# Performance work log

Hardware: AMD Instinct MI355X
Metric: run time of the kernel (lower is better)

The kernel has to match this reference:

```python
import jax, jax.numpy as jnp
import numpy as np

N_SITES = 1024
N_SYMM = 1024
ALPHA_SYMM = 16  # alpha * n_sites / n_symm with alpha=16


def logcosh(x):
    # numerically stable log(cosh(x)) = |x| + log1p(exp(-2|x|)) - log(2)
    ax = jnp.abs(x)
    return ax + jnp.log1p(jnp.exp(-2.0 * ax)) - jnp.log(2.0)


def setup_inputs() -> dict:
    key = jax.random.key(0)
    k1, k2, k3, k4 = jax.random.split(key, 4)
    x_in = jax.random.normal(k1, (4096, N_SITES), dtype=jnp.float32)
    Wsymm = jax.random.normal(k2, (N_SITES, ALPHA_SYMM), dtype=jnp.float32) * 0.1
    bsymm = jax.random.normal(k3, (ALPHA_SYMM,), dtype=jnp.float32) * 0.1
    v_bias = jax.random.normal(k4, (1,), dtype=jnp.float32) * 0.1
    # cyclic translation group: perm_i[k] = (k + i) mod n_sites
    perms = (np.arange(N_SITES)[:, None] + np.arange(N_SITES)[None, :]) % N_SITES
    perms = jnp.asarray(perms, dtype=jnp.int32)  # [n_symm, n_sites]
    return {"x_in": x_in, "Wsymm": Wsymm, "bsymm": bsymm, "v_bias": v_bias, "perms": perms}


def reference(x_in, Wsymm, bsymm, v_bias, perms):
    n_symm, n_sites = perms.shape
    # expand_kernel: kernel[i, j*n_sites + k] = Wsymm[perms[i, k], j]
    # Wsymm[perms] -> [n_symm, n_sites, alpha_symm]; transpose and flatten -> [n_symm, alpha_symm*n_sites]
    kernel = jnp.transpose(Wsymm[perms], (0, 2, 1)).reshape(n_symm, -1)
    # expand_bias: repeat each bsymm[j] n_symm times -> [alpha_symm*n_symm]
    bias = jnp.repeat(bsymm, n_symm)
    y = x_in @ kernel + bias  # [batch, n_hidden]
    y = jnp.sum(logcosh(y), axis=-1)  # [batch]
    y = y + v_bias[0] * jnp.sum(x_in, axis=-1)
    return y
```

## Files before the change

kernel.cpp:

```cpp
#include <hip/hip_runtime.h>
#include <hip/hip_bf16.h>
#include <math.h>

#define LN2F 0.6931471805599453f
#define SCL 9.765625e-4f

typedef __attribute__((ext_vector_type(2))) float f32x2;


#define LSW(s) ((s) ^ (((s) >> 4) & 15))

__device__ __forceinline__ f32x2 mk2(float x, float y) { f32x2 r; r.x = x; r.y = y; return r; }
__device__ __forceinline__ f32x2 crot(f32x2 d) { return mk2(-d.y, d.x); }
__device__ __forceinline__ f32x2 cmul(f32x2 a, f32x2 b) {
  return a.xx * b + mk2(-a.y, a.y) * b.yx;
}
__device__ __forceinline__ f32x2 cmulj(f32x2 a, f32x2 b) {
  return b.xx * a + mk2(b.y, -b.y) * a.yx;
}

__device__ __forceinline__ f32x2 Ctw(int m) {
  switch (m) {
    case 0:   return mk2(1.f, 0.f);
    case 1:   return mk2(0.999981175f, -0.006135885f);
    case 2:   return mk2(0.999924702f, -0.012271538f);
    case 3:   return mk2(0.999830582f, -0.018406730f);
    case 64:  return mk2(0.923879533f, -0.382683432f);
    case 128: return mk2(0.707106781f, -0.707106781f);
    case 192: return mk2(0.382683432f, -0.923879533f);
    case 256: return mk2(0.f, -1.f);
    case 384: return mk2(-0.707106781f, -0.707106781f);
    case 576: return mk2(-0.923879533f, 0.382683432f);
  }
  return mk2(1.f, 0.f);
}

#define BFLY_F(x0,x1,x2,x3,W1,W2,W3,y0,y1,y2,y3) do { \
  f32x2 t0 = x0+x2, t1 = x1+x3, t2 = x0-x2, d_ = x1-x3; \
  f32x2 t3 = mk2(d_.y, -d_.x); \
  y0 = t0+t1; y1 = cmul(t2+t3, W1); \
  y2 = cmul(t0-t1, W2); y3 = cmul(t2-t3, W3); } while(0)

#define BFLY_I(x0,x1,x2,x3,W1,W2,W3,y0,y1,y2,y3) do { \
  f32x2 u1 = cmulj(x1,W1), u2 = cmulj(x2,W2), u3 = cmulj(x3,W3); \
  f32x2 t0 = x0+u2, t1 = u1+u3, t2 = x0-u2, d_ = u1-u3; \
  f32x2 t3 = mk2(-d_.y, d_.x); \
  y0 = t0+t1; y1 = t2+t3; y2 = t0-t1; y3 = t2-t3; } while(0)

#define BFLY_I1(x0,x1,x2,x3,y0,y1,y2,y3) do { \
  f32x2 t0 = x0+x2, t1 = x1+x3, t2 = x0-x2, d_ = x1-x3; \
  f32x2 t3 = mk2(-d_.y, d_.x); \
  y0 = t0+t1; y1 = t2+t3; y2 = t0-t1; y3 = t2-t3; } while(0)

__device__ __forceinline__ float lc(float v) {
  float a = fabsf(v);
  return a + __logf(1.f + __expf(-2.f * a));
}

__global__ void k_twiddle(f32x2* __restrict__ tw) {
  int m = blockIdx.x * 256 + threadIdx.x;
  float th = (float)(2.0 * M_PI / 1024.0) * (float)m;
  tw[m] = mk2(cosf(th), -sinf(th));
}

__global__ __launch_bounds__(256, 3) void k_fft_fwd(
    const float* __restrict__ src, int estride, int rstride,
    const f32x2* __restrict__ tw, f32x2* __restrict__ dst,
    const float* __restrict__ vbias, float* __restrict__ out, int dorow) {
  __shared__ __align__(16) f32x2 fft[4][1024];
  int tid = threadIdx.x, wv = tid >> 6, u = tid & 63;
  int row = blockIdx.x * 4 + wv;
  const float* xr = src + (size_t)row * rstride;
  f32x2* L = fft[wv];
  f32x2 twu = tw[u];
  f32x2 tw4u = tw[4 * u];
  int tp = u & 3;
  f32x2 tw16t = tw[16 * tp], tw64t = tw[64 * tp];

  float vr[4][4]; float rs = 0.f;
  #pragma unroll
  for (int a = 0; a < 4; ++a)
    #pragma unroll
    for (int k = 0; k < 4; ++k) {
      float s = xr[(u + 64 * a + 256 * k) * estride];
      vr[a][k] = s; rs += s;
    }
  f32x2 v[4][4];
  #pragma unroll
  for (int a = 0; a < 4; ++a) {
    float x0 = vr[a][0], x1 = vr[a][1], x2 = vr[a][2], x3 = vr[a][3];
    float t0 = x0 + x2, t1 = x1 + x3, t2 = x0 - x2, dm = x1 - x3;
    f32x2 W1 = cmul(twu, Ctw(64 * a));
    f32x2 W2 = cmul(W1, W1), W3 = cmul(W1, W2);
    v[a][0] = mk2(t0 + t1, 0.f);
    v[a][1] = cmul(mk2(t2, -dm), W1);
    v[a][2] = cmul(mk2(t0 - t1, 0.f), W2);
    v[a][3] = cmul(mk2(t2, dm), W3);
  }
  {
    f32x2 W1 = tw4u, W2 = cmul(W1, W1), W3 = cmul(W1, W2);
    #pragma unroll
    for (int k = 0; k < 4; ++k) {
      f32x2 y0,y1,y2,y3;
      BFLY_F(v[0][k], v[1][k], v[2][k], v[3][k], W1, W2, W3, y0,y1,y2,y3);
      v[0][k]=y0; v[1][k]=y1; v[2][k]=y2; v[3][k]=y3;
    }
  }
  #pragma unroll
  for (int a = 0; a < 4; ++a)
    #pragma unroll
    for (int k = 0; k < 4; ++k)
      L[LSW(u + 64 * a + 256 * k)] = v[a][k];

  int D = u >> 2;
  f32x2 w[4][4];
  #pragma unroll
  for (int c = 0; c < 4; ++c)
    #pragma unroll
    for (int ap = 0; ap < 4; ++ap)
      w[c][ap] = L[LSW(64 * D + 16 * c + 4 * ap + tp)];
  #pragma unroll
  for (int ap = 0; ap < 4; ++ap) {
    f32x2 W1 = cmul(Ctw(64 * ap), tw16t);
    f32x2 W2 = cmul(W1, W1), W3 = cmul(W1, W2);
    f32x2 y0,y1,y2,y3;
    BFLY_F(w[0][ap], w[1][ap], w[2][ap], w[3][ap], W1, W2, W3, y0,y1,y2,y3);
    w[0][ap]=y0; w[1][ap]=y1; w[2][ap]=y2; w[3][ap]=y3;
  }
  {
    f32x2 W1 = tw64t, W2 = cmul(W1, W1), W3 = cmul(W1, W2);
    #pragma unroll
    for (int c = 0; c < 4; ++c) {
      f32x2 y0,y1,y2,y3;
      BFLY_F(w[c][0], w[c][1], w[c][2], w[c][3], W1, W2, W3, y0,y1,y2,y3);
      w[c][0]=y0; w[c][1]=y1; w[c][2]=y2; w[c][3]=y3;
    }
  }
  #pragma unroll
  for (int c = 0; c < 4; ++c)
    #pragma unroll
    for (int ap = 0; ap < 4; ++ap)
      L[LSW(64 * D + 16 * c + 4 * ap + tp)] = w[c][ap];

  f32x2* drow = dst + (size_t)row * 1024;
  #pragma unroll
  for (int j = 0; j < 4; ++j) {
    f32x2 z0 = L[LSW(16 * u + 4 * j)];
    f32x2 z1 = L[LSW(16 * u + 4 * j + 1)];
    f32x2 z2 = L[LSW(16 * u + 4 * j + 2)];
    f32x2 z3 = L[LSW(16 * u + 4 * j + 3)];
    f32x2 t0 = z0+z2, t1 = z1+z3, t2 = z0-z2, d = z1-z3;
    f32x2 t3 = mk2(d.y, -d.x);
    f32x2 y0 = t0+t1, y1 = t2+t3, y2 = t0-t1, y3 = t2-t3;
    float4* dp = (float4*)(drow + 16 * u + 4 * j);
    dp[0] = make_float4(y0.x, y0.y, y1.x, y1.y);
    dp[1] = make_float4(y2.x, y2.y, y3.x, y3.y);
  }
  if (dorow) {
    #pragma unroll
    for (int m = 32; m; m >>= 1) rs += __shfl_down(rs, m);
    if (u == 0) out[row] = vbias[0] * rs;
  }
}


#define PW(M, XA, XB, ZA, ZB) do { \
  float4 qa = W0p[M], qb = W1p[M]; \
  f32x2 g1 = cmulj(mk2(qa.x,qa.y), XA); \
  f32x2 g2 = cmulj(mk2(qb.x,qb.y), XA); \
  ZA = (g1 + crot(g2)) * SCL; \
  g1 = cmulj(mk2(qa.z,qa.w), XB); \
  g2 = cmulj(mk2(qb.z,qb.w), XB); \
  ZB = (g1 + crot(g2)) * SCL; } while(0)

#define QP_A(P, LB) do { \
  const float4* W0p = (const float4*)(Wfs + (size_t)(2*(P)) * 1024 + s16); \
  const float4* W1p = (const float4*)(Wfs + (size_t)(2*(P) + 1) * 1024 + s16); \
  f32x2 z0,z1,z2,z3,z4,z5,z6,z7,z8,z9,z10,z11,z12,z13,z14,z15; \
  PW(0, xr0, xr1, z0, z1);   PW(1, xr2, xr3, z2, z3); \
  PW(2, xr4, xr5, z4, z5);   PW(3, xr6, xr7, z6, z7); \
  PW(4, xr8, xr9, z8, z9);   PW(5, xr10, xr11, z10, z11); \
  PW(6, xr12, xr13, z12, z13); PW(7, xr14, xr15, z14, z15); \
   \
  BFLY_I1(z0,z1,z2,z3, z0,z1,z2,z3); \
  BFLY_I1(z4,z5,z6,z7, z4,z5,z6,z7); \
  BFLY_I1(z8,z9,z10,z11, z8,z9,z10,z11); \
  BFLY_I1(z12,z13,z14,z15, z12,z13,z14,z15); \
   \
  BFLY_I1(z0,z4,z8,z12, z0,z4,z8,z12); \
  BFLY_I(z1,z5,z9,z13, Ctw(64),Ctw(128),Ctw(192), z1,z5,z9,z13); \
  BFLY_I(z2,z6,z10,z14, Ctw(128),Ctw(256),Ctw(384), z2,z6,z10,z14); \
  BFLY_I(z3,z7,z11,z15, Ctw(192),Ctw(384),Ctw(576), z3,z7,z11,z15); \
  (LB)[LSW(s16+0)]=z0;   (LB)[LSW(s16+1)]=z1;   (LB)[LSW(s16+2)]=z2;   (LB)[LSW(s16+3)]=z3; \
  (LB)[LSW(s16+4)]=z4;   (LB)[LSW(s16+5)]=z5;   (LB)[LSW(s16+6)]=z6;   (LB)[LSW(s16+7)]=z7; \
  (LB)[LSW(s16+8)]=z8;   (LB)[LSW(s16+9)]=z9;   (LB)[LSW(s16+10)]=z10; (LB)[LSW(s16+11)]=z11; \
  (LB)[LSW(s16+12)]=z12; (LB)[LSW(s16+13)]=z13; (LB)[LSW(s16+14)]=z14; (LB)[LSW(s16+15)]=z15; \
} while(0)

#define QP_B(LB) do { \
  f32x2 w00,w01,w02,w03,w10,w11,w12,w13,w20,w21,w22,w23,w30,w31,w32,w33; \
  w00 = (LB)[LSW(sB+0)];   w01 = (LB)[LSW(sB+64)];  w02 = (LB)[LSW(sB+128)]; w03 = (LB)[LSW(sB+192)]; \
  w10 = (LB)[LSW(sB+16)];  w11 = (LB)[LSW(sB+80)];  w12 = (LB)[LSW(sB+144)]; w13 = (LB)[LSW(sB+208)]; \
  w20 = (LB)[LSW(sB+32)];  w21 = (LB)[LSW(sB+96)];  w22 = (LB)[LSW(sB+160)]; w23 = (LB)[LSW(sB+224)]; \
  w30 = (LB)[LSW(sB+48)];  w31 = (LB)[LSW(sB+112)]; w32 = (LB)[LSW(sB+176)]; w33 = (LB)[LSW(sB+240)]; \
  BFLY_I(w00,w10,w20,w30, TB1,TB2,TB3, w00,w10,w20,w30); \
  BFLY_I(w01,w11,w21,w31, TB1,TB2,TB3, w01,w11,w21,w31); \
  BFLY_I(w02,w12,w22,w32, TB1,TB2,TB3, w02,w12,w22,w32); \
  BFLY_I(w03,w13,w23,w33, TB1,TB2,TB3, w03,w13,w23,w33); \
  BFLY_I(w00,w01,w02,w03, TC10,TC20,TC30, w00,w01,w02,w03); \
  BFLY_I(w10,w11,w12,w13, TC11,TC21,TC31, w10,w11,w12,w13); \
  BFLY_I(w20,w21,w22,w23, TC12,TC22,TC32, w20,w21,w22,w23); \
  BFLY_I(w30,w31,w32,w33, TC13,TC23,TC33, w30,w31,w32,w33); \
  (LB)[LSW(sB+0)]=w00;   (LB)[LSW(sB+64)]=w01;  (LB)[LSW(sB+128)]=w02; (LB)[LSW(sB+192)]=w03; \
  (LB)[LSW(sB+16)]=w10;  (LB)[LSW(sB+80)]=w11;  (LB)[LSW(sB+144)]=w12; (LB)[LSW(sB+208)]=w13; \
  (LB)[LSW(sB+32)]=w20;  (LB)[LSW(sB+96)]=w21;  (LB)[LSW(sB+160)]=w22; (LB)[LSW(sB+224)]=w23; \
  (LB)[LSW(sB+48)]=w30;  (LB)[LSW(sB+112)]=w31; (LB)[LSW(sB+176)]=w32; (LB)[LSW(sB+240)]=w33; \
} while(0)

#define QPC_PH(LB, I, T1, T2, T3, BS0, BS1) do { \
  f32x2 c0 = (LB)[LSW(s4+(I))],     c1 = (LB)[LSW(s4+(I)+256)]; \
  f32x2 c2 = (LB)[LSW(s4+(I)+512)], c3 = (LB)[LSW(s4+(I)+768)]; \
  BFLY_I(c0,c1,c2,c3,T1,T2,T3,c0,c1,c2,c3); \
  a0 += lc(c0.x+(BS0)) + lc(c0.y+(BS1)); \
  a1 += lc(c1.x+(BS0)) + lc(c1.y+(BS1)); \
  a2 += lc(c2.x+(BS0)) + lc(c2.y+(BS1)); \
  a3 += lc(c3.x+(BS0)) + lc(c3.y+(BS1)); } while(0)

#define QP_C(LB, BS0, BS1) do { \
  QPC_PH(LB, 0, TD10, TD20, TD30, BS0, BS1); \
  QPC_PH(LB, 1, TD11, TD21, TD31, BS0, BS1); \
  QPC_PH(LB, 2, TD12, TD22, TD32, BS0, BS1); \
  QPC_PH(LB, 3, TD13, TD23, TD33, BS0, BS1); } while(0)

__global__ __launch_bounds__(512, 4) void k_corr(
    const f32x2* __restrict__ X, const f32x2* __restrict__ Wfs,
    const float* __restrict__ bs, const f32x2* __restrict__ tw,
    float* __restrict__ out) {
  __shared__ __align__(16) f32x2 LBW[8][1024];
  __shared__ float red[8];
  int tid = threadIdx.x, wv = tid >> 6, u = tid & 63;
  int b = blockIdx.x;
  f32x2* L0 = LBW[wv];
  f32x2 tw4u = tw[4 * u];
  int t = u & 15;
  f32x2 tw16t = tw[16 * t], tw4t = tw[4 * t];
  int s16 = 16 * u;
  int sB = 256 * (u >> 4) + t;
  int s4 = 4 * u;

  f32x2 xr0,xr1,xr2,xr3,xr4,xr5,xr6,xr7,xr8,xr9,xr10,xr11,xr12,xr13,xr14,xr15;
  {
    const float4* Xp = (const float4*)(X + (size_t)b * 1024 + s16);
    float4 q;
    q = Xp[0]; xr0  = mk2(q.x,q.y); xr1  = mk2(q.z,q.w);
    q = Xp[1]; xr2  = mk2(q.x,q.y); xr3  = mk2(q.z,q.w);
    q = Xp[2]; xr4  = mk2(q.x,q.y); xr5  = mk2(q.z,q.w);
    q = Xp[3]; xr6  = mk2(q.x,q.y); xr7  = mk2(q.z,q.w);
    q = Xp[4]; xr8  = mk2(q.x,q.y); xr9  = mk2(q.z,q.w);
    q = Xp[5]; xr10 = mk2(q.x,q.y); xr11 = mk2(q.z,q.w);
    q = Xp[6]; xr12 = mk2(q.x,q.y); xr13 = mk2(q.z,q.w);
    q = Xp[7]; xr14 = mk2(q.x,q.y); xr15 = mk2(q.z,q.w);
  }
  float bs0 = bs[2*wv], bs1 = bs[2*wv+1];

  QP_A(wv, L0);

  f32x2 TB1 = tw16t, TB2 = cmul(TB1,TB1), TB3 = cmul(TB1,TB2);
  f32x2 TC10 = tw4t,               TC20 = cmul(TC10,TC10), TC30 = cmul(TC10,TC20);
  f32x2 TC11 = cmul(tw4t,Ctw(64)),  TC21 = cmul(TC11,TC11), TC31 = cmul(TC11,TC21);
  f32x2 TC12 = cmul(tw4t,Ctw(128)), TC22 = cmul(TC12,TC12), TC32 = cmul(TC12,TC22);
  f32x2 TC13 = cmul(tw4t,Ctw(192)), TC23 = cmul(TC13,TC13), TC33 = cmul(TC13,TC23);

  QP_B(L0);

  f32x2 TD10 = tw4u,              TD20 = cmul(TD10,TD10), TD30 = cmul(TD10,TD20);
  f32x2 TD11 = cmul(tw4u,Ctw(1)), TD21 = cmul(TD11,TD11), TD31 = cmul(TD11,TD21);
  f32x2 TD12 = cmul(tw4u,Ctw(2)), TD22 = cmul(TD12,TD12), TD32 = cmul(TD12,TD22);
  f32x2 TD13 = cmul(tw4u,Ctw(3)), TD23 = cmul(TD13,TD13), TD33 = cmul(TD13,TD23);

  float a0 = 0.f, a1 = 0.f, a2 = 0.f, a3 = 0.f;
  QP_C(L0, bs0, bs1);

  float acc = (a0 + a1) + (a2 + a3);
  #pragma unroll
  for (int m = 32; m; m >>= 1) acc += __shfl_down(acc, m);
  if (u == 0) red[wv] = acc;
  __syncthreads();
  if (tid == 0) {
    float s = ((red[0] + red[1]) + (red[2] + red[3]))
            + ((red[4] + red[5]) + (red[6] + red[7]));
    out[b] += s - 16384.f * LN2F;
  }
}

__global__ void k_naive(const float* __restrict__ x, const float* __restrict__ W,
                        const float* __restrict__ bs, const float* __restrict__ vb,
                        float* __restrict__ out) {
  int b = blockIdx.x;
  __shared__ float xs[1024];
  __shared__ float red[256];
  int t = threadIdx.x;
  float xsum = 0.f;
  for (int i = t; i < 1024; i += 256) { float v = x[(size_t)b * 1024 + i]; xs[i] = v; xsum += v; }
  __syncthreads();
  float tot = vb[0] * xsum;
  for (int h = t; h < 16384; h += 256) {
    int j = h >> 10, kh = h & 1023;
    float a = bs[j];
    for (int i = 0; i < 1024; ++i) a += xs[i] * W[((i + kh) & 1023) * 16 + j];
    float ax = fabsf(a);
    tot += ax + __logf(1.f + __expf(-2.f * ax)) - LN2F;
  }
  red[t] = tot;
  __syncthreads();
  for (int s2 = 128; s2; s2 >>= 1) { if (t < s2) red[t] += red[t + s2]; __syncthreads(); }
  if (t == 0) out[b] = red[0];
}

extern "C" void kernel_launch(void* const* d_in, const int* in_sizes, int n_in,
                              void* d_out, int out_size, void* d_ws, size_t ws_size,
                              hipStream_t stream) {
  const float* x  = (const float*)d_in[0];
  const float* W  = (const float*)d_in[1];
  const float* bs = (const float*)d_in[2];
  const float* vb = (const float*)d_in[3];
  float* out = (float*)d_out;

  size_t need = 8192 + 131072 + (size_t)4096 * 1024 * 8;
  if (ws_size < need) {
    k_naive<<<4096, 256, 0, stream>>>(x, W, bs, vb, out);
    return;
  }
  f32x2* tw  = (f32x2*)d_ws;
  f32x2* Wfs = (f32x2*)((char*)d_ws + 8192);
  f32x2* X   = (f32x2*)((char*)d_ws + 8192 + 131072);

  k_twiddle<<<4, 256, 0, stream>>>(tw);
  k_fft_fwd<<<4, 256, 0, stream>>>(W, 16, 1, tw, Wfs, vb, out, 0);
  k_fft_fwd<<<1024, 256, 0, stream>>>(x, 1, 1024, tw, X, vb, out, 1);
  k_corr<<<4096, 512, 0, stream>>>(X, Wfs, bs, tw, out);
}
```

Measured before the change: 138.5 us.

## Pad LDS layout, fold FFT scale into W, and use log2-domain logcosh

Replaces the XOR-swizzled LDS indexing in the correlation kernel with a padded layout (row stride 17/272, plus a u>>2 offset) and precomputed per-lane base pointers, which removes the per-access swizzle arithmetic. The 1/1024 inverse-FFT scale moves into the one-time W spectrum kernel, taking a multiply off every pointwise product. logcosh is rewritten in base 2 using a packed abs via max, a vector accumulator for the linear term and a single ln2 factor at the end. This cuts per-element ALU work, at the cost of more shared memory per block and slightly different rounding.

```diff
diff --git a/kernel.cpp b/kernel.cpp
--- a/kernel.cpp
+++ b/kernel.cpp
@@ -4,6 +4,7 @@
 
 #define LN2F 0.6931471805599453f
 #define SCL 9.765625e-4f
+#define TWO_OVER_LN2 2.885390081777927f
 
 typedef __attribute__((ext_vector_type(2))) float f32x2;
 
@@ -17,6 +18,13 @@
 }
 __device__ __forceinline__ f32x2 cmulj(f32x2 a, f32x2 b) {
   return b.xx * a + mk2(b.y, -b.y) * a.yx;
+}
+__device__ __forceinline__ f32x2 vmax2(f32x2 a, f32x2 b) {
+#if __has_builtin(__builtin_elementwise_max)
+  return __builtin_elementwise_max(a, b);
+#else
+  return mk2(fmaxf(a.x, b.x), fmaxf(a.y, b.y));
+#endif
 }
 
 __device__ __forceinline__ f32x2 Ctw(int m) {
@@ -52,11 +60,6 @@
   f32x2 t3 = mk2(-d_.y, d_.x); \
   y0 = t0+t1; y1 = t2+t3; y2 = t0-t1; y3 = t2-t3; } while(0)
 
-__device__ __forceinline__ float lc(float v) {
-  float a = fabsf(v);
-  return a + __logf(1.f + __expf(-2.f * a));
-}
-
 __global__ void k_twiddle(f32x2* __restrict__ tw) {
   int m = blockIdx.x * 256 + threadIdx.x;
   float th = (float)(2.0 * M_PI / 1024.0) * (float)m;
@@ -65,7 +68,7 @@
 
 __global__ __launch_bounds__(256, 3) void k_fft_fwd(
     const float* __restrict__ src, int estride, int rstride,
-    const f32x2* __restrict__ tw, f32x2* __restrict__ dst,
+    const f32x2* __restrict__ tw, f32x2* __restrict__ dst, float scale,
     const float* __restrict__ vbias, float* __restrict__ out, int dorow) {
   __shared__ __align__(16) f32x2 fft[4][1024];
   int tid = threadIdx.x, wv = tid >> 6, u = tid & 63;
@@ -151,7 +154,7 @@
     f32x2 z3 = L[LSW(16 * u + 4 * j + 3)];
     f32x2 t0 = z0+z2, t1 = z1+z3, t2 = z0-z2, d = z1-z3;
     f32x2 t3 = mk2(d.y, -d.x);
-    f32x2 y0 = t0+t1, y1 = t2+t3, y2 = t0-t1, y3 = t2-t3;
+    f32x2 y0 = (t0+t1)*scale, y1 = (t2+t3)*scale, y2 = (t0-t1)*scale, y3 = (t2-t3)*scale;
     float4* dp = (float4*)(drow + 16 * u + 4 * j);
     dp[0] = make_float4(y0.x, y0.y, y1.x, y1.y);
     dp[1] = make_float4(y2.x, y2.y, y3.x, y3.y);
@@ -168,12 +171,12 @@
   float4 qa = W0p[M], qb = W1p[M]; \
   f32x2 g1 = cmulj(mk2(qa.x,qa.y), XA); \
   f32x2 g2 = cmulj(mk2(qb.x,qb.y), XA); \
-  ZA = (g1 + crot(g2)) * SCL; \
+  ZA = g1 + crot(g2); \
   g1 = cmulj(mk2(qa.z,qa.w), XB); \
   g2 = cmulj(mk2(qb.z,qb.w), XB); \
-  ZB = (g1 + crot(g2)) * SCL; } while(0)
-
-#define QP_A(P, LB) do { \
+  ZB = g1 + crot(g2); } while(0)
+
+#define QP_A(P, LPA) do { \
   const float4* W0p = (const float4*)(Wfs + (size_t)(2*(P)) * 1024 + s16); \
   const float4* W1p = (const float4*)(Wfs + (size_t)(2*(P) + 1) * 1024 + s16); \
   f32x2 z0,z1,z2,z3,z4,z5,z6,z7,z8,z9,z10,z11,z12,z13,z14,z15; \
@@ -181,28 +184,26 @@
   PW(2, xr4, xr5, z4, z5);   PW(3, xr6, xr7, z6, z7); \
   PW(4, xr8, xr9, z8, z9);   PW(5, xr10, xr11, z10, z11); \
   PW(6, xr12, xr13, z12, z13); PW(7, xr14, xr15, z14, z15); \
-   \
   BFLY_I1(z0,z1,z2,z3, z0,z1,z2,z3); \
   BFLY_I1(z4,z5,z6,z7, z4,z5,z6,z7); \
   BFLY_I1(z8,z9,z10,z11, z8,z9,z10,z11); \
   BFLY_I1(z12,z13,z14,z15, z12,z13,z14,z15); \
-   \
   BFLY_I1(z0,z4,z8,z12, z0,z4,z8,z12); \
   BFLY_I(z1,z5,z9,z13, Ctw(64),Ctw(128),Ctw(192), z1,z5,z9,z13); \
   BFLY_I(z2,z6,z10,z14, Ctw(128),Ctw(256),Ctw(384), z2,z6,z10,z14); \
   BFLY_I(z3,z7,z11,z15, Ctw(192),Ctw(384),Ctw(576), z3,z7,z11,z15); \
-  (LB)[LSW(s16+0)]=z0;   (LB)[LSW(s16+1)]=z1;   (LB)[LSW(s16+2)]=z2;   (LB)[LSW(s16+3)]=z3; \
-  (LB)[LSW(s16+4)]=z4;   (LB)[LSW(s16+5)]=z5;   (LB)[LSW(s16+6)]=z6;   (LB)[LSW(s16+7)]=z7; \
-  (LB)[LSW(s16+8)]=z8;   (LB)[LSW(s16+9)]=z9;   (LB)[LSW(s16+10)]=z10; (LB)[LSW(s16+11)]=z11; \
-  (LB)[LSW(s16+12)]=z12; (LB)[LSW(s16+13)]=z13; (LB)[LSW(s16+14)]=z14; (LB)[LSW(s16+15)]=z15; \
+  (LPA)[0]=z0;   (LPA)[1]=z1;   (LPA)[2]=z2;   (LPA)[3]=z3; \
+  (LPA)[4]=z4;   (LPA)[5]=z5;   (LPA)[6]=z6;   (LPA)[7]=z7; \
+  (LPA)[8]=z8;   (LPA)[9]=z9;   (LPA)[10]=z10; (LPA)[11]=z11; \
+  (LPA)[12]=z12; (LPA)[13]=z13; (LPA)[14]=z14; (LPA)[15]=z15; \
 } while(0)
 
-#define QP_B(LB) do { \
+#define QP_B(LPB) do { \
   f32x2 w00,w01,w02,w03,w10,w11,w12,w13,w20,w21,w22,w23,w30,w31,w32,w33; \
-  w00 = (LB)[LSW(sB+0)];   w01 = (LB)[LSW(sB+64)];  w02 = (LB)[LSW(sB+128)]; w03 = (LB)[LSW(sB+192)]; \
-  w10 = (LB)[LSW(sB+16)];  w11 = (LB)[LSW(sB+80)];  w12 = (LB)[LSW(sB+144)]; w13 = (LB)[LSW(sB+208)]; \
-  w20 = (LB)[LSW(sB+32)];  w21 = (LB)[LSW(sB+96)];  w22 = (LB)[LSW(sB+160)]; w23 = (LB)[LSW(sB+224)]; \
-  w30 = (LB)[LSW(sB+48)];  w31 = (LB)[LSW(sB+112)]; w32 = (LB)[LSW(sB+176)]; w33 = (LB)[LSW(sB+240)]; \
+  w00 = (LPB)[0];   w01 = (LPB)[68];  w02 = (LPB)[136]; w03 = (LPB)[204]; \
+  w10 = (LPB)[17];  w11 = (LPB)[85];  w12 = (LPB)[153]; w13 = (LPB)[221]; \
+  w20 = (LPB)[34];  w21 = (LPB)[102]; w22 = (LPB)[170]; w23 = (LPB)[238]; \
+  w30 = (LPB)[51];  w31 = (LPB)[119]; w32 = (LPB)[187]; w33 = (LPB)[255]; \
   BFLY_I(w00,w10,w20,w30, TB1,TB2,TB3, w00,w10,w20,w30); \
   BFLY_I(w01,w11,w21,w31, TB1,TB2,TB3, w01,w11,w21,w31); \
   BFLY_I(w02,w12,w22,w32, TB1,TB2,TB3, w02,w12,w22,w32); \
@@ -211,42 +212,48 @@
   BFLY_I(w10,w11,w12,w13, TC11,TC21,TC31, w10,w11,w12,w13); \
   BFLY_I(w20,w21,w22,w23, TC12,TC22,TC32, w20,w21,w22,w23); \
   BFLY_I(w30,w31,w32,w33, TC13,TC23,TC33, w30,w31,w32,w33); \
-  (LB)[LSW(sB+0)]=w00;   (LB)[LSW(sB+64)]=w01;  (LB)[LSW(sB+128)]=w02; (LB)[LSW(sB+192)]=w03; \
-  (LB)[LSW(sB+16)]=w10;  (LB)[LSW(sB+80)]=w11;  (LB)[LSW(sB+144)]=w12; (LB)[LSW(sB+208)]=w13; \
-  (LB)[LSW(sB+32)]=w20;  (LB)[LSW(sB+96)]=w21;  (LB)[LSW(sB+160)]=w22; (LB)[LSW(sB+224)]=w23; \
-  (LB)[LSW(sB+48)]=w30;  (LB)[LSW(sB+112)]=w31; (LB)[LSW(sB+176)]=w32; (LB)[LSW(sB+240)]=w33; \
+  (LPB)[0]=w00;   (LPB)[68]=w01;  (LPB)[136]=w02; (LPB)[204]=w03; \
+  (LPB)[17]=w10;  (LPB)[85]=w11;  (LPB)[153]=w12; (LPB)[221]=w13; \
+  (LPB)[34]=w20;  (LPB)[102]=w21; (LPB)[170]=w22; (LPB)[238]=w23; \
+  (LPB)[51]=w30;  (LPB)[119]=w31; (LPB)[187]=w32; (LPB)[255]=w33; \
 } while(0)
 
-#define QPC_PH(LB, I, T1, T2, T3, BS0, BS1) do { \
-  f32x2 c0 = (LB)[LSW(s4+(I))],     c1 = (LB)[LSW(s4+(I)+256)]; \
-  f32x2 c2 = (LB)[LSW(s4+(I)+512)], c3 = (LB)[LSW(s4+(I)+768)]; \
+#define LCACC(C) do { \
+  f32x2 t2 = (C) + bias2; \
+  f32x2 a2 = vmax2(t2, -t2); \
+  f32x2 u2 = a2 * TWO_OVER_LN2; \
+  accL += __log2f(1.f + exp2f(-u2.x)); \
+  accL += __log2f(1.f + exp2f(-u2.y)); \
+  accU += u2; } while(0)
+
+#define QPC_PH(LPC, I, T1, T2, T3) do { \
+  f32x2 c0 = (LPC)[(I)],     c1 = (LPC)[(I)+272]; \
+  f32x2 c2 = (LPC)[(I)+544], c3 = (LPC)[(I)+816]; \
   BFLY_I(c0,c1,c2,c3,T1,T2,T3,c0,c1,c2,c3); \
-  a0 += lc(c0.x+(BS0)) + lc(c0.y+(BS1)); \
-  a1 += lc(c1.x+(BS0)) + lc(c1.y+(BS1)); \
-  a2 += lc(c2.x+(BS0)) + lc(c2.y+(BS1)); \
-  a3 += lc(c3.x+(BS0)) + lc(c3.y+(BS1)); } while(0)
-
-#define QP_C(LB, BS0, BS1) do { \
-  QPC_PH(LB, 0, TD10, TD20, TD30, BS0, BS1); \
-  QPC_PH(LB, 1, TD11, TD21, TD31, BS0, BS1); \
-  QPC_PH(LB, 2, TD12, TD22, TD32, BS0, BS1); \
-  QPC_PH(LB, 3, TD13, TD23, TD33, BS0, BS1); } while(0)
+  LCACC(c0); LCACC(c1); LCACC(c2); LCACC(c3); } while(0)
+
+#define QP_C(LPC) do { \
+  QPC_PH(LPC, 0, TD10, TD20, TD30); \
+  QPC_PH(LPC, 1, TD11, TD21, TD31); \
+  QPC_PH(LPC, 2, TD12, TD22, TD32); \
+  QPC_PH(LPC, 3, TD13, TD23, TD33); } while(0)
 
 __global__ __launch_bounds__(512, 4) void k_corr(
     const f32x2* __restrict__ X, const f32x2* __restrict__ Wfs,
     const float* __restrict__ bs, const f32x2* __restrict__ tw,
     float* __restrict__ out) {
-  __shared__ __align__(16) f32x2 LBW[8][1024];
+  __shared__ __align__(16) f32x2 LBW[8][1088];
   __shared__ float red[8];
   int tid = threadIdx.x, wv = tid >> 6, u = tid & 63;
   int b = blockIdx.x;
-  f32x2* L0 = LBW[wv];
+  f32x2* L = LBW[wv];
+  f32x2* LPA = L + 17 * u;
+  f32x2* LPB = L + 272 * (u >> 4) + (u & 15);
+  f32x2* LPC = L + 4 * u + (u >> 2);
   f32x2 tw4u = tw[4 * u];
   int t = u & 15;
   f32x2 tw16t = tw[16 * t], tw4t = tw[4 * t];
   int s16 = 16 * u;
-  int sB = 256 * (u >> 4) + t;
-  int s4 = 4 * u;
 
   f32x2 xr0,xr1,xr2,xr3,xr4,xr5,xr6,xr7,xr8,xr9,xr10,xr11,xr12,xr13,xr14,xr15;
   {
@@ -261,9 +268,9 @@
     q = Xp[6]; xr12 = mk2(q.x,q.y); xr13 = mk2(q.z,q.w);
     q = Xp[7]; xr14 = mk2(q.x,q.y); xr15 = mk2(q.z,q.w);
   }
-  float bs0 = bs[2*wv], bs1 = bs[2*wv+1];
-
-  QP_A(wv, L0);
+  f32x2 bias2 = mk2(bs[2*wv], bs[2*wv+1]);
+
+  QP_A(wv, LPA);
 
   f32x2 TB1 = tw16t, TB2 = cmul(TB1,TB1), TB3 = cmul(TB1,TB2);
   f32x2 TC10 = tw4t,               TC20 = cmul(TC10,TC10), TC30 = cmul(TC10,TC20);
@@ -271,17 +278,18 @@
   f32x2 TC12 = cmul(tw4t,Ctw(128)), TC22 = cmul(TC12,TC12), TC32 = cmul(TC12,TC22);
   f32x2 TC13 = cmul(tw4t,Ctw(192)), TC23 = cmul(TC13,TC13), TC33 = cmul(TC13,TC23);
 
-  QP_B(L0);
+  QP_B(LPB);
 
   f32x2 TD10 = tw4u,              TD20 = cmul(TD10,TD10), TD30 = cmul(TD10,TD20);
   f32x2 TD11 = cmul(tw4u,Ctw(1)), TD21 = cmul(TD11,TD11), TD31 = cmul(TD11,TD21);
   f32x2 TD12 = cmul(tw4u,Ctw(2)), TD22 = cmul(TD12,TD12), TD32 = cmul(TD12,TD22);
   f32x2 TD13 = cmul(tw4u,Ctw(3)), TD23 = cmul(TD13,TD13), TD33 = cmul(TD13,TD23);
 
-  float a0 = 0.f, a1 = 0.f, a2 = 0.f, a3 = 0.f;
-  QP_C(L0, bs0, bs1);
-
-  float acc = (a0 + a1) + (a2 + a3);
+  float accL = 0.f;
+  f32x2 accU = mk2(0.f, 0.f);
+  QP_C(LPC);
+
+  float acc = accL + 0.5f * (accU.x + accU.y);
   #pragma unroll
   for (int m = 32; m; m >>= 1) acc += __shfl_down(acc, m);
   if (u == 0) red[wv] = acc;
@@ -289,7 +297,7 @@
   if (tid == 0) {
     float s = ((red[0] + red[1]) + (red[2] + red[3]))
             + ((red[4] + red[5]) + (red[6] + red[7]));
-    out[b] += s - 16384.f * LN2F;
+    out[b] += LN2F * (s - 16384.f);
   }
 }
 
@@ -336,7 +344,7 @@
   f32x2* X   = (f32x2*)((char*)d_ws + 8192 + 131072);
 
   k_twiddle<<<4, 256, 0, stream>>>(tw);
-  k_fft_fwd<<<4, 256, 0, stream>>>(W, 16, 1, tw, Wfs, vb, out, 0);
-  k_fft_fwd<<<1024, 256, 0, stream>>>(x, 1, 1024, tw, X, vb, out, 1);
+  k_fft_fwd<<<4, 256, 0, stream>>>(W, 16, 1, tw, Wfs, SCL, vb, out, 0);
+  k_fft_fwd<<<1024, 256, 0, stream>>>(x, 1, 1024, tw, X, 1.0f, vb, out, 1);
   k_corr<<<4096, 512, 0, stream>>>(X, Wfs, bs, tw, out);
 }
```

Measured after the change: 139.6 us. About the same (+0.8%).
